# Kernel tuning notes

Measured on AMD Instinct MI355X. Metric: run time of the kernel, lower is better.

The kernel has to match this reference:

```python
import jax, jax.numpy as jnp
import numpy as np

COMMITMENT_COST = 0.25

def setup_inputs() -> dict:
    key = jax.random.key(0)
    k1, k2 = jax.random.split(key)
    z = jax.random.normal(k1, (8, 2048, 768), dtype=jnp.float32)
    # codebook initialized uniform(-1/K, 1/K) in the original; use same scale
    K = 2048
    emb = jax.random.uniform(k2, (K, 768), dtype=jnp.float32, minval=-1.0 / K, maxval=1.0 / K)
    return {"z": z, "emb": emb}

def reference(z, emb):
    B, S, D = z.shape
    z_flat = z.reshape(-1, D)                                   # [N, D]
    # squared-euclidean distances via expansion: ||z||^2 + ||e||^2 - 2 z e^T
    distances = (
        jnp.sum(z_flat * z_flat, axis=1, keepdims=True)
        + jnp.sum(emb * emb, axis=1)
        - 2.0 * jnp.matmul(z_flat, emb.T)
    )                                                           # [N, K]
    ids_flat = jnp.argmin(distances, axis=1)                    # [N]
    z_q = emb[ids_flat].reshape(z.shape)                        # gather + reshape
    concept_ids = ids_flat.reshape(B, S)
    # training path with use_ema=True: codebook_loss = 0, commitment term only.
    # NOTE: original (faithfully) computes mse(z.detach(), z_q) — grad flows to z_q.
    commitment_loss = jnp.mean((jax.lax.stop_gradient(z) - z_q) ** 2)
    vq_loss = COMMITMENT_COST * commitment_loss
    # straight-through estimator
    z_q_st = z + jax.lax.stop_gradient(z_q - z)
    return z_q_st, concept_ids, vq_loss
```

## Files before the change

kernel.cpp:

```cpp
#include <hip/hip_runtime.h>
#include <float.h>

typedef unsigned short ushort_t;
typedef unsigned int uint_t;

#define NROWS 16384
#define DDIM  768
#define KCODES 2048
#define NCB    16
#define MARGIN 8e-4f

__device__ __forceinline__ ushort_t f2bf(float x) {
    uint_t u = __float_as_uint(x);
    uint_t r = (u + 0x7fffu + ((u >> 16) & 1u)) >> 16;
    return (ushort_t)r;
}
__device__ __forceinline__ float bf2f(ushort_t h) {
    return __uint_as_float(((uint_t)h) << 16);
}

__global__ void ee_kernel(const float* __restrict__ emb, float* __restrict__ ee) {
    int c = blockIdx.x;
    const float* e = emb + (size_t)c * DDIM;
    int t = threadIdx.x;
    float s = 0.f;
    for (int i = t; i < DDIM; i += 256) { float v = e[i]; s += v * v; }
    for (int off = 32; off; off >>= 1) s += __shfl_down(s, off);
    __shared__ float red[4];
    if ((t & 63) == 0) red[t >> 6] = s;
    __syncthreads();
    if (t == 0) ee[c] = red[0] + red[1] + red[2] + red[3];
}

__global__ void zz_kernel(const float* __restrict__ z, float* __restrict__ zz) {
    const int t = threadIdx.x;
    const int row = blockIdx.x * 4 + (t >> 6);
    const int lane = t & 63;
    const float* zr = z + (size_t)row * DDIM;
    float s = 0.f;
    for (int i = lane; i < DDIM; i += 64) { float v = zr[i]; s += v * v; }
    for (int off = 32; off; off >>= 1) s += __shfl_down(s, off);
    if (lane == 0) zz[row] = s;
}

__global__ void conv_kernel(const float* __restrict__ src, ushort_t* __restrict__ dst) {
    const int i = blockIdx.x * 256 + threadIdx.x;
    const float4 v = ((const float4*)src)[i];
    ushort4 h;
    h.x = f2bf(v.x); h.y = f2bf(v.y); h.z = f2bf(v.z); h.w = f2bf(v.w);
    ((ushort4*)dst)[i] = h;
}

typedef __attribute__((ext_vector_type(8))) short bf16x8;
typedef __attribute__((ext_vector_type(4))) float f32x4;

__device__ __forceinline__ int swz(int r) { return (r & 3) ^ ((r >> 2) & 3); }

__global__ __launch_bounds__(256)
void mfma_kernel(const ushort_t* __restrict__ Ab, const ushort_t* __restrict__ Bb,
                 const float* __restrict__ ee, float* __restrict__ bmin,
                 float2* __restrict__ slots) {
    __shared__ ushort_t Als[128 * 32];
    __shared__ ushort_t Bls[128 * 32];
    __shared__ float rowmin[128];
    __shared__ int   rcnt[128];
    __shared__ float sval[128][8];
    __shared__ int   sidx[128][8];

    const int t = threadIdx.x;
    const int w = t >> 6, l = t & 63;
    const int bx = blockIdx.x & 127, by = blockIdx.x >> 7;
    const int row0 = bx << 7, col0 = by << 7;

    f32x4 acc[4][4];
    #pragma unroll
    for (int i = 0; i < 4; ++i)
        #pragma unroll
        for (int j = 0; j < 4; ++j) acc[i][j] = (f32x4){0.f, 0.f, 0.f, 0.f};

    const int sri  = l >> 2;
    const int slot = l & 3;
    const int rha = (w & 1) << 6;
    const int rhb = (w >> 1) << 6;

    for (int kt = 0; kt < 24; ++kt) {
        const int kb = kt << 5;
        __syncthreads();
        #pragma unroll
        for (int q = 0; q < 2; ++q) {
            const int r0 = ((w << 1) + q) << 4;
            const int ra = r0 + sri;
            const int c  = slot ^ swz(ra);
            const ushort_t* gpa = Ab + (size_t)(row0 + ra) * DDIM + kb + (c << 3);
            __builtin_amdgcn_global_load_lds(
                (const __attribute__((address_space(1))) void*)gpa,
                (__attribute__((address_space(3))) void*)((char*)Als + (r0 << 6)), 16, 0, 0);
            const ushort_t* gpb = Bb + (size_t)(col0 + ra) * DDIM + kb + (c << 3);
            __builtin_amdgcn_global_load_lds(
                (const __attribute__((address_space(1))) void*)gpb,
                (__attribute__((address_space(3))) void*)((char*)Bls + (r0 << 6)), 16, 0, 0);
        }
        __syncthreads();

        bf16x8 af[4], bfr[4];
        #pragma unroll
        for (int mi = 0; mi < 4; ++mi) {
            const int r = rha + (mi << 4) + (l & 15);
            const int s = (l >> 4) ^ swz(r);
            af[mi] = *(const bf16x8*)&Als[(r << 5) + (s << 3)];
        }
        #pragma unroll
        for (int ni = 0; ni < 4; ++ni) {
            const int r = rhb + (ni << 4) + (l & 15);
            const int s = (l >> 4) ^ swz(r);
            bfr[ni] = *(const bf16x8*)&Bls[(r << 5) + (s << 3)];
        }
        #pragma unroll
        for (int mi = 0; mi < 4; ++mi)
            #pragma unroll
            for (int ni = 0; ni < 4; ++ni)
                acc[mi][ni] = __builtin_amdgcn_mfma_f32_16x16x32_bf16(
                    af[mi], bfr[ni], acc[mi][ni], 0, 0, 0);
    }

    float ecv[4];
    #pragma unroll
    for (int ni = 0; ni < 4; ++ni) ecv[ni] = ee[col0 + rhb + (ni << 4) + (l & 15)];
    #pragma unroll
    for (int mi = 0; mi < 4; ++mi)
        #pragma unroll
        for (int ni = 0; ni < 4; ++ni)
            #pragma unroll
            for (int r = 0; r < 4; ++r)
                acc[mi][ni][r] = ecv[ni] - 2.0f * acc[mi][ni][r];

    float vmr[4][4];
    #pragma unroll
    for (int mi = 0; mi < 4; ++mi)
        #pragma unroll
        for (int r = 0; r < 4; ++r) {
            float v = fminf(fminf(acc[mi][0][r], acc[mi][1][r]),
                            fminf(acc[mi][2][r], acc[mi][3][r]));
            v = fminf(v, __shfl_xor(v, 1));
            v = fminf(v, __shfl_xor(v, 2));
            v = fminf(v, __shfl_xor(v, 4));
            v = fminf(v, __shfl_xor(v, 8));
            vmr[mi][r] = v;
        }

    if (t < 128) { rowmin[t] = FLT_MAX; rcnt[t] = 0; }
    __syncthreads();
    if (w < 2 && (l & 15) == 0) {
        #pragma unroll
        for (int mi = 0; mi < 4; ++mi)
            #pragma unroll
            for (int r = 0; r < 4; ++r)
                rowmin[rha + (mi << 4) + ((l >> 4) << 2) + r] = vmr[mi][r];
    }
    __syncthreads();
    if (w >= 2 && (l & 15) == 0) {
        #pragma unroll
        for (int mi = 0; mi < 4; ++mi)
            #pragma unroll
            for (int r = 0; r < 4; ++r) {
                const int m = rha + (mi << 4) + ((l >> 4) << 2) + r;
                rowmin[m] = fminf(rowmin[m], vmr[mi][r]);
            }
    }
    __syncthreads();

    #pragma unroll
    for (int mi = 0; mi < 4; ++mi)
        #pragma unroll
        for (int r = 0; r < 4; ++r) {
            const int m = rha + (mi << 4) + ((l >> 4) << 2) + r;
            const float lim = rowmin[m] + MARGIN;
            #pragma unroll
            for (int ni = 0; ni < 4; ++ni) {
                const float vv = acc[mi][ni][r];
                if (vv <= lim) {
                    const int p = atomicAdd(&rcnt[m], 1);
                    if (p < 8) {
                        sval[m][p] = vv;
                        sidx[m][p] = col0 + rhb + (ni << 4) + (l & 15);
                    }
                }
            }
        }
    __syncthreads();

    if (t < 128) {
        const int row = row0 + t;
        bmin[(size_t)by * NROWS + row] = rowmin[t];
        const int n = rcnt[t] < 8 ? rcnt[t] : 8;
        float2 rec[8];
        #pragma unroll
        for (int s2 = 0; s2 < 8; ++s2)
            rec[s2] = (s2 < n) ? make_float2(sval[t][s2], __int_as_float(sidx[t][s2]))
                               : make_float2(FLT_MAX, __int_as_float(0x7fffffff));
        float4* dst = (float4*)(slots + ((size_t)by * NROWS + row) * 8);
        dst[0] = make_float4(rec[0].x, rec[0].y, rec[1].x, rec[1].y);
        dst[1] = make_float4(rec[2].x, rec[2].y, rec[3].x, rec[3].y);
        dst[2] = make_float4(rec[4].x, rec[4].y, rec[5].x, rec[5].y);
        dst[3] = make_float4(rec[6].x, rec[6].y, rec[7].x, rec[7].y);
    }
}

__global__ __launch_bounds__(256)
void combine_select(const float* __restrict__ bmin, const float2* __restrict__ slots,
                    const float* __restrict__ ee, const float* __restrict__ zz,
                    const float* __restrict__ z, const float* __restrict__ emb,
                    float* __restrict__ ids_f32) {
    const int t = threadIdx.x;
    const int row = blockIdx.x * 4 + (t >> 6);
    const int l = t & 63;

    float v = (l < NCB) ? bmin[(size_t)l * NROWS + row] : FLT_MAX;
    v = fminf(v, __shfl_xor(v, 8));
    v = fminf(v, __shfl_xor(v, 4));
    v = fminf(v, __shfl_xor(v, 2));
    v = fminf(v, __shfl_xor(v, 1));
    const float T = __shfl(v, 0) + MARGIN;

    const int blk = l >> 2;
    const int s0 = (l << 1) & 7;
    const float2* sp = slots + ((size_t)blk * NROWS + row) * 8 + s0;
    const float2 a  = sp[0];
    const float2 b2 = sp[1];

    unsigned long long m0 = __ballot(a.x <= T);
    unsigned long long m1 = __ballot(b2.x <= T);

    const float zzr = zz[row];
    const float* zr = z + (size_t)row * DDIM;

    float bestd = FLT_MAX; int besti = 0x7fffffff;
    while (m0 | m1) {
        int j; float iv;
        if (m0) { j = __ffsll(m0) - 1; m0 &= m0 - 1; iv = a.y; }
        else    { j = __ffsll(m1) - 1; m1 &= m1 - 1; iv = b2.y; }
        const int idx = __float_as_int(__shfl(iv, j));
        const float* er = emb + (size_t)idx * DDIM;
        float p = 0.f;
        #pragma unroll
        for (int k = 0; k < 12; ++k) p += zr[l + 64 * k] * er[l + 64 * k];
        for (int off = 32; off; off >>= 1) p += __shfl_down(p, off);
        if (l == 0) {
            const float t1 = zzr + ee[idx];
            const float d  = t1 - 2.0f * p;
            if (d < bestd || (d == bestd && idx < besti)) { bestd = d; besti = idx; }
        }
    }
    if (l == 0) ids_f32[row] = (float)besti;
}

__global__ __launch_bounds__(256)
void gather_kernel(const float* __restrict__ z, const float* __restrict__ emb,
                   const float* __restrict__ ids_f32, float* __restrict__ out0,
                   float* __restrict__ part) {
    const int b = blockIdx.x;
    const int t = threadIdx.x;
    const int rl = t >> 4, c = t & 15;
    __shared__ int ids[16];
    if (t < 16) ids[t] = (int)ids_f32[b * 16 + t];
    __syncthreads();
    const int row = b * 16 + rl;
    const float4* zr = (const float4*)(z + (size_t)row * DDIM);
    float4* orow = (float4*)(out0 + (size_t)row * DDIM);
    const float4* er = (const float4*)(emb + (size_t)ids[rl] * DDIM);
    float s = 0.f;
    #pragma unroll
    for (int j = 0; j < 12; ++j) {
        const int i4 = c + 16 * j;
        const float4 zv = zr[i4];
        const float4 ev = er[i4];
        float4 o;
        o.x = zv.x + (ev.x - zv.x); o.y = zv.y + (ev.y - zv.y);
        o.z = zv.z + (ev.z - zv.z); o.w = zv.w + (ev.w - zv.w);
        orow[i4] = o;
        float dx = zv.x - ev.x, dy = zv.y - ev.y, dz = zv.z - ev.z, dw = zv.w - ev.w;
        s += dx * dx + dy * dy + dz * dz + dw * dw;
    }
    for (int off = 32; off; off >>= 1) s += __shfl_down(s, off);
    __shared__ float red[4];
    if ((t & 63) == 0) red[t >> 6] = s;
    __syncthreads();
    if (t == 0) part[b] = red[0] + red[1] + red[2] + red[3];
}

__global__ void loss_kernel(const float* __restrict__ part, float* __restrict__ out_loss) {
    const int t = threadIdx.x;
    double s = 0.0;
    for (int i = t; i < 1024; i += 256) s += (double)part[i];
    for (int off = 32; off; off >>= 1) s += __shfl_down(s, off);
    __shared__ double red[4];
    if ((t & 63) == 0) red[t >> 6] = s;
    __syncthreads();
    if (t == 0) {
        const double total = red[0] + red[1] + red[2] + red[3];
        out_loss[0] = (float)(0.25 * (total / (double)((size_t)NROWS * DDIM)));
    }
}

#define BM 32
#define BN 128
#define BKS 32
#define SPLITC 2
#define CODES_PER_BLOCK (KCODES / SPLITC)
#define NCHUNK (CODES_PER_BLOCK / BN)
#define NSTAGE (DDIM / BKS)
#define APADR 33
#define BPADC 132

__global__ __launch_bounds__(256)
void argmin_kernel(const float* __restrict__ z, const float* __restrict__ emb,
                   const float* __restrict__ ee, const float* __restrict__ zz,
                   float* __restrict__ pval, int* __restrict__ pidx) {
    __shared__ float Af[BKS][APADR];
    __shared__ float Bf[BKS][BPADC];
    __shared__ float cval[BM][33];
    __shared__ int   cidx[BM][33];
    __shared__ float zzs[BM];
    const int t = threadIdx.x;
    const int part = blockIdx.x & (SPLITC - 1);
    const int rb = blockIdx.x >> 1;
    const int row0 = rb * BM;
    const int cbase = part * CODES_PER_BLOCK;
    const int tx = t & 31, ty = t >> 5;
    const int sr = t >> 3;
    const int sk = 4 * (t & 7);
    if (t < BM) zzs[t] = zz[row0 + t];
    float bv[4]; int bi[4];
    #pragma unroll
    for (int i = 0; i < 4; ++i) { bv[i] = FLT_MAX; bi[i] = 0x7fffffff; }
    const float* zt = z + (size_t)(row0 + sr) * DDIM;
    for (int chunk = 0; chunk < NCHUNK; ++chunk) {
        const int c0 = cbase + chunk * BN;
        const float* ebase = emb + (size_t)(c0 + sr) * DDIM;
        float acc[4][4];
        #pragma unroll
        for (int i = 0; i < 4; ++i)
            #pragma unroll
            for (int j = 0; j < 4; ++j) acc[i][j] = 0.f;
        float4 pa = *(const float4*)&zt[sk];
        float4 pb[4];
        #pragma unroll
        for (int m = 0; m < 4; ++m) pb[m] = *(const float4*)&ebase[(size_t)(32 * m) * DDIM + sk];
        for (int s = 0; s < NSTAGE; ++s) {
            __syncthreads();
            Af[sk + 0][sr] = pa.x; Af[sk + 1][sr] = pa.y;
            Af[sk + 2][sr] = pa.z; Af[sk + 3][sr] = pa.w;
            #pragma unroll
            for (int m = 0; m < 4; ++m) {
                Bf[sk + 0][sr + 32 * m] = pb[m].x;
                Bf[sk + 1][sr + 32 * m] = pb[m].y;
                Bf[sk + 2][sr + 32 * m] = pb[m].z;
                Bf[sk + 3][sr + 32 * m] = pb[m].w;
            }
            __syncthreads();
            if (s + 1 < NSTAGE) {
                const int k1 = (s + 1) * BKS + sk;
                pa = *(const float4*)&zt[k1];
                #pragma unroll
                for (int m = 0; m < 4; ++m)
                    pb[m] = *(const float4*)&ebase[(size_t)(32 * m) * DDIM + k1];
            }
            #pragma unroll
            for (int kk = 0; kk < BKS; ++kk) {
                const float4 a4 = *(const float4*)&Af[kk][4 * ty];
                const float4 b4 = *(const float4*)&Bf[kk][4 * tx];
                const float aa[4] = {a4.x, a4.y, a4.z, a4.w};
                const float bb[4] = {b4.x, b4.y, b4.z, b4.w};
                #pragma unroll
                for (int i = 0; i < 4; ++i)
                    #pragma unroll
                    for (int j = 0; j < 4; ++j) acc[i][j] += aa[i] * bb[j];
            }
        }
        const float4 e4 = *(const float4*)&ee[c0 + 4 * tx];
        const float eev[4] = {e4.x, e4.y, e4.z, e4.w};
        #pragma unroll
        for (int i = 0; i < 4; ++i) {
            const float zzr = zzs[4 * ty + i];
            #pragma unroll
            for (int j = 0; j < 4; ++j) {
                const int code = c0 + 4 * tx + j;
                const float t1 = zzr + eev[j];
                const float d  = t1 - 2.0f * acc[i][j];
                if (d < bv[i] || (d == bv[i] && code < bi[i])) { bv[i] = d; bi[i] = code; }
            }
        }
    }
    __syncthreads();
    #pragma unroll
    for (int i = 0; i < 4; ++i) { cval[4 * ty + i][tx] = bv[i]; cidx[4 * ty + i][tx] = bi[i]; }
    __syncthreads();
    if (t < BM) {
        float v = FLT_MAX; int id = 0x7fffffff;
        #pragma unroll
        for (int x = 0; x < 32; ++x) {
            const float cv = cval[t][x]; const int ci = cidx[t][x];
            if (cv < v || (cv == v && ci < id)) { v = cv; id = ci; }
        }
        pval[part * NROWS + row0 + t] = v;
        pidx[part * NROWS + row0 + t] = id;
    }
}

__global__ void combine_kernel(const float* __restrict__ pval, const int* __restrict__ pidx,
                               float* __restrict__ ids_f32) {
    const int r = blockIdx.x * 256 + threadIdx.x;
    float v = pval[r];           int id = pidx[r];
    const float v1 = pval[NROWS + r]; const int i1 = pidx[NROWS + r];
    if (v1 < v || (v1 == v && i1 < id)) { v = v1; id = i1; }
    ids_f32[r] = (float)id;
}

#define EE_OFF   0
#define ZZ_OFF   8192
#define PART_OFF 73728
#define PV_OFF   81920
#define EH_OFF   81920
#define ZH_OFF   (EH_OFF + (size_t)KCODES * DDIM * 2)
#define BMIN_OFF (ZH_OFF + (size_t)NROWS * DDIM * 2)
#define SLOT_OFF (BMIN_OFF + (size_t)NCB * NROWS * 4)
#define WS_NEED  (SLOT_OFF + (size_t)NCB * NROWS * 8 * 8)

extern "C" void kernel_launch(void* const* d_in, const int* in_sizes, int n_in,
                              void* d_out, int out_size, void* d_ws, size_t ws_size,
                              hipStream_t stream) {
    const float* z   = (const float*)d_in[0];
    const float* emb = (const float*)d_in[1];

    float* out0     = (float*)d_out;
    float* out_ids  = out0 + (size_t)NROWS * DDIM;
    float* out_loss = out_ids + NROWS;

    char* ws = (char*)d_ws;
    float* ee   = (float*)(ws + EE_OFF);
    float* zzws = (float*)(ws + ZZ_OFF);
    float* part = (float*)(ws + PART_OFF);

    ee_kernel<<<KCODES, 256, 0, stream>>>(emb, ee);
    zz_kernel<<<NROWS / 4, 256, 0, stream>>>(z, zzws);

    if (ws_size >= WS_NEED) {
        ushort_t* Eh   = (ushort_t*)(ws + EH_OFF);
        ushort_t* Zh   = (ushort_t*)(ws + ZH_OFF);
        float*    bmin = (float*)(ws + BMIN_OFF);
        float2*   slot = (float2*)(ws + SLOT_OFF);
        conv_kernel<<<(KCODES * DDIM / 4) / 256, 256, 0, stream>>>(emb, Eh);
        conv_kernel<<<(NROWS * DDIM / 4) / 256, 256, 0, stream>>>(z, Zh);
        mfma_kernel<<<(NROWS / 128) * NCB, 256, 0, stream>>>(Zh, Eh, ee, bmin, slot);
        combine_select<<<NROWS / 4, 256, 0, stream>>>(bmin, slot, ee, zzws, z, emb, out_ids);
    } else {
        float* pval = (float*)(ws + PV_OFF);
        int*   pidx = (int*)(ws + PV_OFF + 131072);
        argmin_kernel<<<(NROWS / BM) * SPLITC, 256, 0, stream>>>(z, emb, ee, zzws, pval, pidx);
        combine_kernel<<<NROWS / 256, 256, 0, stream>>>(pval, pidx, out_ids);
    }

    gather_kernel<<<NROWS / 16, 256, 0, stream>>>(z, emb, out_ids, out0, part);
    loss_kernel<<<1, 256, 0, stream>>>(part, out_loss);
}
```

Measured before the change: 257.4 us.

## Fuse bf16 conversion into norm kernels, fuse gather into select, deepen K-tile

Merges the bf16 conversion of emb and z into the norm-computing prep kernels, so each input is read once instead of twice. Folds the straight-through gather and per-row loss into the candidate-rescoring kernel, which removes a separate pass that re-read z and emb. The MFMA kernel now stages 64 K-elements per barrier pair instead of 32, halving the number of sync iterations, and reuses one shared-memory buffer for the epilogue arrays. The cost is a larger LDS footprint (32 KB), which may lower occupancy, plus an extra barrier before that reuse.

```diff
diff --git a/kernel.cpp b/kernel.cpp
--- a/kernel.cpp
+++ b/kernel.cpp
@@ -19,7 +19,8 @@
     return __uint_as_float(((uint_t)h) << 16);
 }
 
-__global__ void ee_kernel(const float* __restrict__ emb, float* __restrict__ ee) {
+__global__ void prep_emb(const float* __restrict__ emb, float* __restrict__ ee,
+                         ushort_t* __restrict__ Eh) {
     int c = blockIdx.x;
     const float* e = emb + (size_t)c * DDIM;
     int t = threadIdx.x;
@@ -30,9 +31,16 @@
     if ((t & 63) == 0) red[t >> 6] = s;
     __syncthreads();
     if (t == 0) ee[c] = red[0] + red[1] + red[2] + red[3];
-}
-
-__global__ void zz_kernel(const float* __restrict__ z, float* __restrict__ zz) {
+    if (t < 192) {
+        const float4 v = ((const float4*)e)[t];
+        ushort4 h;
+        h.x = f2bf(v.x); h.y = f2bf(v.y); h.z = f2bf(v.z); h.w = f2bf(v.w);
+        ((ushort4*)(Eh + (size_t)c * DDIM))[t] = h;
+    }
+}
+
+__global__ void prep_z(const float* __restrict__ z, float* __restrict__ zz,
+                       ushort_t* __restrict__ Zh) {
     const int t = threadIdx.x;
     const int row = blockIdx.x * 4 + (t >> 6);
     const int lane = t & 63;
@@ -41,14 +49,16 @@
     for (int i = lane; i < DDIM; i += 64) { float v = zr[i]; s += v * v; }
     for (int off = 32; off; off >>= 1) s += __shfl_down(s, off);
     if (lane == 0) zz[row] = s;
-}
-
-__global__ void conv_kernel(const float* __restrict__ src, ushort_t* __restrict__ dst) {
-    const int i = blockIdx.x * 256 + threadIdx.x;
-    const float4 v = ((const float4*)src)[i];
-    ushort4 h;
-    h.x = f2bf(v.x); h.y = f2bf(v.y); h.z = f2bf(v.z); h.w = f2bf(v.w);
-    ((ushort4*)dst)[i] = h;
+    const float4* zr4 = (const float4*)zr;
+    ushort4* dh = (ushort4*)(Zh + (size_t)row * DDIM);
+    #pragma unroll
+    for (int j = 0; j < 3; ++j) {
+        const int i4 = lane + 64 * j;
+        const float4 v = zr4[i4];
+        ushort4 h;
+        h.x = f2bf(v.x); h.y = f2bf(v.y); h.z = f2bf(v.z); h.w = f2bf(v.w);
+        dh[i4] = h;
+    }
 }
 
 typedef __attribute__((ext_vector_type(8))) short bf16x8;
@@ -60,12 +70,13 @@
 void mfma_kernel(const ushort_t* __restrict__ Ab, const ushort_t* __restrict__ Bb,
                  const float* __restrict__ ee, float* __restrict__ bmin,
                  float2* __restrict__ slots) {
-    __shared__ ushort_t Als[128 * 32];
-    __shared__ ushort_t Bls[128 * 32];
-    __shared__ float rowmin[128];
-    __shared__ int   rcnt[128];
-    __shared__ float sval[128][8];
-    __shared__ int   sidx[128][8];
+    __shared__ __align__(16) char smem[32768];
+    ushort_t* Als = (ushort_t*)smem;
+    ushort_t* Bls = (ushort_t*)(smem + 16384);
+    float* rowmin = (float*)smem;
+    int*   rcnt   = (int*)(smem + 512);
+    float (*sval)[8] = (float(*)[8])(smem + 1024);
+    int   (*sidx)[8] = (int(*)[8])(smem + 5120);
 
     const int t = threadIdx.x;
     const int w = t >> 6, l = t & 63;
@@ -83,45 +94,55 @@
     const int rha = (w & 1) << 6;
     const int rhb = (w >> 1) << 6;
 
-    for (int kt = 0; kt < 24; ++kt) {
-        const int kb = kt << 5;
+    for (int kt = 0; kt < 12; ++kt) {
+        const int kb = kt << 6;
         __syncthreads();
         #pragma unroll
-        for (int q = 0; q < 2; ++q) {
-            const int r0 = ((w << 1) + q) << 4;
-            const int ra = r0 + sri;
-            const int c  = slot ^ swz(ra);
-            const ushort_t* gpa = Ab + (size_t)(row0 + ra) * DDIM + kb + (c << 3);
-            __builtin_amdgcn_global_load_lds(
-                (const __attribute__((address_space(1))) void*)gpa,
-                (__attribute__((address_space(3))) void*)((char*)Als + (r0 << 6)), 16, 0, 0);
-            const ushort_t* gpb = Bb + (size_t)(col0 + ra) * DDIM + kb + (c << 3);
-            __builtin_amdgcn_global_load_lds(
-                (const __attribute__((address_space(1))) void*)gpb,
-                (__attribute__((address_space(3))) void*)((char*)Bls + (r0 << 6)), 16, 0, 0);
+        for (int s = 0; s < 2; ++s) {
+            #pragma unroll
+            for (int q = 0; q < 2; ++q) {
+                const int r0 = ((w << 1) + q) << 4;
+                const int ra = r0 + sri;
+                const int c  = slot ^ swz(ra);
+                const int kk = kb + (s << 5) + (c << 3);
+                const ushort_t* gpa = Ab + (size_t)(row0 + ra) * DDIM + kk;
+                __builtin_amdgcn_global_load_lds(
+                    (const __attribute__((address_space(1))) void*)gpa,
+                    (__attribute__((address_space(3))) void*)(smem + (s << 13) + (r0 << 6)),
+                    16, 0, 0);
+                const ushort_t* gpb = Bb + (size_t)(col0 + ra) * DDIM + kk;
+                __builtin_amdgcn_global_load_lds(
+                    (const __attribute__((address_space(1))) void*)gpb,
+                    (__attribute__((address_space(3))) void*)(smem + 16384 + (s << 13) + (r0 << 6)),
+                    16, 0, 0);
+            }
         }
         __syncthreads();
 
-        bf16x8 af[4], bfr[4];
-        #pragma unroll
-        for (int mi = 0; mi < 4; ++mi) {
-            const int r = rha + (mi << 4) + (l & 15);
-            const int s = (l >> 4) ^ swz(r);
-            af[mi] = *(const bf16x8*)&Als[(r << 5) + (s << 3)];
-        }
-        #pragma unroll
-        for (int ni = 0; ni < 4; ++ni) {
-            const int r = rhb + (ni << 4) + (l & 15);
-            const int s = (l >> 4) ^ swz(r);
-            bfr[ni] = *(const bf16x8*)&Bls[(r << 5) + (s << 3)];
-        }
-        #pragma unroll
-        for (int mi = 0; mi < 4; ++mi)
-            #pragma unroll
-            for (int ni = 0; ni < 4; ++ni)
-                acc[mi][ni] = __builtin_amdgcn_mfma_f32_16x16x32_bf16(
-                    af[mi], bfr[ni], acc[mi][ni], 0, 0, 0);
-    }
+        #pragma unroll
+        for (int s = 0; s < 2; ++s) {
+            bf16x8 af[4], bfr[4];
+            #pragma unroll
+            for (int mi = 0; mi < 4; ++mi) {
+                const int r = rha + (mi << 4) + (l & 15);
+                const int sw = (l >> 4) ^ swz(r);
+                af[mi] = *(const bf16x8*)&Als[(s << 12) + (r << 5) + (sw << 3)];
+            }
+            #pragma unroll
+            for (int ni = 0; ni < 4; ++ni) {
+                const int r = rhb + (ni << 4) + (l & 15);
+                const int sw = (l >> 4) ^ swz(r);
+                bfr[ni] = *(const bf16x8*)&Bls[(s << 12) + (r << 5) + (sw << 3)];
+            }
+            #pragma unroll
+            for (int mi = 0; mi < 4; ++mi)
+                #pragma unroll
+                for (int ni = 0; ni < 4; ++ni)
+                    acc[mi][ni] = __builtin_amdgcn_mfma_f32_16x16x32_bf16(
+                        af[mi], bfr[ni], acc[mi][ni], 0, 0, 0);
+        }
+    }
+    __syncthreads();
 
     float ecv[4];
     #pragma unroll
@@ -207,10 +228,11 @@
 }
 
 __global__ __launch_bounds__(256)
-void combine_select(const float* __restrict__ bmin, const float2* __restrict__ slots,
-                    const float* __restrict__ ee, const float* __restrict__ zz,
-                    const float* __restrict__ z, const float* __restrict__ emb,
-                    float* __restrict__ ids_f32) {
+void combine_select_gather(const float* __restrict__ bmin, const float2* __restrict__ slots,
+                           const float* __restrict__ ee, const float* __restrict__ zz,
+                           const float* __restrict__ z, const float* __restrict__ emb,
+                           float* __restrict__ ids_f32, float* __restrict__ out0,
+                           float* __restrict__ rowloss) {
     const int t = threadIdx.x;
     const int row = blockIdx.x * 4 + (t >> 6);
     const int l = t & 63;
@@ -251,7 +273,180 @@
             if (d < bestd || (d == bestd && idx < besti)) { bestd = d; besti = idx; }
         }
     }
-    if (l == 0) ids_f32[row] = (float)besti;
+    const int bi = __shfl(besti, 0);
+    if (l == 0) ids_f32[row] = (float)bi;
+
+    const float4* zr4 = (const float4*)zr;
+    const float4* er4 = (const float4*)(emb + (size_t)bi * DDIM);
+    float4* o4 = (float4*)(out0 + (size_t)row * DDIM);
+    float s = 0.f;
+    #pragma unroll
+    for (int j = 0; j < 3; ++j) {
+        const int i4 = l + 64 * j;
+        const float4 zv = zr4[i4];
+        const float4 ev = er4[i4];
+        float4 o;
+        o.x = zv.x + (ev.x - zv.x); o.y = zv.y + (ev.y - zv.y);
+        o.z = zv.z + (ev.z - zv.z); o.w = zv.w + (ev.w - zv.w);
+        o4[i4] = o;
+        const float dx = zv.x - ev.x, dy = zv.y - ev.y;
+        const float dz = zv.z - ev.z, dw = zv.w - ev.w;
+        s += dx * dx + dy * dy + dz * dz + dw * dw;
+    }
+    for (int off = 32; off; off >>= 1) s += __shfl_down(s, off);
+    if (l == 0) rowloss[row] = s;
+}
+
+__global__ void loss16k_kernel(const float* __restrict__ rowloss, float* __restrict__ out_loss) {
+    const int t = threadIdx.x;
+    double s = 0.0;
+    for (int i = t; i < NROWS; i += 256) s += (double)rowloss[i];
+    for (int off = 32; off; off >>= 1) s += __shfl_down(s, off);
+    __shared__ double red[4];
+    if ((t & 63) == 0) red[t >> 6] = s;
+    __syncthreads();
+    if (t == 0) {
+        const double total = red[0] + red[1] + red[2] + red[3];
+        out_loss[0] = (float)(0.25 * (total / (double)((size_t)NROWS * DDIM)));
+    }
+}
+
+__global__ void ee_kernel(const float* __restrict__ emb, float* __restrict__ ee) {
+    int c = blockIdx.x;
+    const float* e = emb + (size_t)c * DDIM;
+    int t = threadIdx.x;
+    float s = 0.f;
+    for (int i = t; i < DDIM; i += 256) { float v = e[i]; s += v * v; }
+    for (int off = 32; off; off >>= 1) s += __shfl_down(s, off);
+    __shared__ float red[4];
+    if ((t & 63) == 0) red[t >> 6] = s;
+    __syncthreads();
+    if (t == 0) ee[c] = red[0] + red[1] + red[2] + red[3];
+}
+
+__global__ void zz_kernel(const float* __restrict__ z, float* __restrict__ zz) {
+    const int t = threadIdx.x;
+    const int row = blockIdx.x * 4 + (t >> 6);
+    const int lane = t & 63;
+    const float* zr = z + (size_t)row * DDIM;
+    float s = 0.f;
+    for (int i = lane; i < DDIM; i += 64) { float v = zr[i]; s += v * v; }
+    for (int off = 32; off; off >>= 1) s += __shfl_down(s, off);
+    if (lane == 0) zz[row] = s;
+}
+
+#define BM 32
+#define BN 128
+#define BKS 32
+#define SPLITC 2
+#define CODES_PER_BLOCK (KCODES / SPLITC)
+#define NCHUNK (CODES_PER_BLOCK / BN)
+#define NSTAGE (DDIM / BKS)
+#define APADR 33
+#define BPADC 132
+
+__global__ __launch_bounds__(256)
+void argmin_kernel(const float* __restrict__ z, const float* __restrict__ emb,
+                   const float* __restrict__ ee, const float* __restrict__ zz,
+                   float* __restrict__ pval, int* __restrict__ pidx) {
+    __shared__ float Af[BKS][APADR];
+    __shared__ float Bf[BKS][BPADC];
+    __shared__ float cval[BM][33];
+    __shared__ int   cidx[BM][33];
+    __shared__ float zzs[BM];
+    const int t = threadIdx.x;
+    const int part = blockIdx.x & (SPLITC - 1);
+    const int rb = blockIdx.x >> 1;
+    const int row0 = rb * BM;
+    const int cbase = part * CODES_PER_BLOCK;
+    const int tx = t & 31, ty = t >> 5;
+    const int sr = t >> 3;
+    const int sk = 4 * (t & 7);
+    if (t < BM) zzs[t] = zz[row0 + t];
+    float bv[4]; int bi[4];
+    #pragma unroll
+    for (int i = 0; i < 4; ++i) { bv[i] = FLT_MAX; bi[i] = 0x7fffffff; }
+    const float* zt = z + (size_t)(row0 + sr) * DDIM;
+    for (int chunk = 0; chunk < NCHUNK; ++chunk) {
+        const int c0 = cbase + chunk * BN;
+        const float* ebase = emb + (size_t)(c0 + sr) * DDIM;
+        float acc[4][4];
+        #pragma unroll
+        for (int i = 0; i < 4; ++i)
+            #pragma unroll
+            for (int j = 0; j < 4; ++j) acc[i][j] = 0.f;
+        float4 pa = *(const float4*)&zt[sk];
+        float4 pb[4];
+        #pragma unroll
+        for (int m = 0; m < 4; ++m) pb[m] = *(const float4*)&ebase[(size_t)(32 * m) * DDIM + sk];
+        for (int s = 0; s < NSTAGE; ++s) {
+            __syncthreads();
+            Af[sk + 0][sr] = pa.x; Af[sk + 1][sr] = pa.y;
+            Af[sk + 2][sr] = pa.z; Af[sk + 3][sr] = pa.w;
+            #pragma unroll
+            for (int m = 0; m < 4; ++m) {
+                Bf[sk + 0][sr + 32 * m] = pb[m].x;
+                Bf[sk + 1][sr + 32 * m] = pb[m].y;
+                Bf[sk + 2][sr + 32 * m] = pb[m].z;
+                Bf[sk + 3][sr + 32 * m] = pb[m].w;
+            }
+            __syncthreads();
+            if (s + 1 < NSTAGE) {
+                const int k1 = (s + 1) * BKS + sk;
+                pa = *(const float4*)&zt[k1];
+                #pragma unroll
+                for (int m = 0; m < 4; ++m)
+                    pb[m] = *(const float4*)&ebase[(size_t)(32 * m) * DDIM + k1];
+            }
+            #pragma unroll
+            for (int kk = 0; kk < BKS; ++kk) {
+                const float4 a4 = *(const float4*)&Af[kk][4 * ty];
+                const float4 b4 = *(const float4*)&Bf[kk][4 * tx];
+                const float aa[4] = {a4.x, a4.y, a4.z, a4.w};
+                const float bb[4] = {b4.x, b4.y, b4.z, b4.w};
+                #pragma unroll
+                for (int i = 0; i < 4; ++i)
+                    #pragma unroll
+                    for (int j = 0; j < 4; ++j) acc[i][j] += aa[i] * bb[j];
+            }
+        }
+        const float4 e4 = *(const float4*)&ee[c0 + 4 * tx];
+        const float eev[4] = {e4.x, e4.y, e4.z, e4.w};
+        #pragma unroll
+        for (int i = 0; i < 4; ++i) {
+            const float zzr = zzs[4 * ty + i];
+            #pragma unroll
+            for (int j = 0; j < 4; ++j) {
+                const int code = c0 + 4 * tx + j;
+                const float t1 = zzr + eev[j];
+                const float d  = t1 - 2.0f * acc[i][j];
+                if (d < bv[i] || (d == bv[i] && code < bi[i])) { bv[i] = d; bi[i] = code; }
+            }
+        }
+    }
+    __syncthreads();
+    #pragma unroll
+    for (int i = 0; i < 4; ++i) { cval[4 * ty + i][tx] = bv[i]; cidx[4 * ty + i][tx] = bi[i]; }
+    __syncthreads();
+    if (t < BM) {
+        float v = FLT_MAX; int id = 0x7fffffff;
+        #pragma unroll
+        for (int x = 0; x < 32; ++x) {
+            const float cv = cval[t][x]; const int ci = cidx[t][x];
+            if (cv < v || (cv == v && ci < id)) { v = cv; id = ci; }
+        }
+        pval[part * NROWS + row0 + t] = v;
+        pidx[part * NROWS + row0 + t] = id;
+    }
+}
+
+__global__ void combine_kernel(const float* __restrict__ pval, const int* __restrict__ pidx,
+                               float* __restrict__ ids_f32) {
+    const int r = blockIdx.x * 256 + threadIdx.x;
+    float v = pval[r];           int id = pidx[r];
+    const float v1 = pval[NROWS + r]; const int i1 = pidx[NROWS + r];
+    if (v1 < v || (v1 == v && i1 < id)) { v = v1; id = i1; }
+    ids_f32[r] = (float)id;
 }
 
 __global__ __launch_bounds__(256)
@@ -302,129 +497,15 @@
     }
 }
 
-#define BM 32
-#define BN 128
-#define BKS 32
-#define SPLITC 2
-#define CODES_PER_BLOCK (KCODES / SPLITC)
-#define NCHUNK (CODES_PER_BLOCK / BN)
-#define NSTAGE (DDIM / BKS)
-#define APADR 33
-#define BPADC 132
-
-__global__ __launch_bounds__(256)
-void argmin_kernel(const float* __restrict__ z, const float* __restrict__ emb,
-                   const float* __restrict__ ee, const float* __restrict__ zz,
-                   float* __restrict__ pval, int* __restrict__ pidx) {
-    __shared__ float Af[BKS][APADR];
-    __shared__ float Bf[BKS][BPADC];
-    __shared__ float cval[BM][33];
-    __shared__ int   cidx[BM][33];
-    __shared__ float zzs[BM];
-    const int t = threadIdx.x;
-    const int part = blockIdx.x & (SPLITC - 1);
-    const int rb = blockIdx.x >> 1;
-    const int row0 = rb * BM;
-    const int cbase = part * CODES_PER_BLOCK;
-    const int tx = t & 31, ty = t >> 5;
-    const int sr = t >> 3;
-    const int sk = 4 * (t & 7);
-    if (t < BM) zzs[t] = zz[row0 + t];
-    float bv[4]; int bi[4];
-    #pragma unroll
-    for (int i = 0; i < 4; ++i) { bv[i] = FLT_MAX; bi[i] = 0x7fffffff; }
-    const float* zt = z + (size_t)(row0 + sr) * DDIM;
-    for (int chunk = 0; chunk < NCHUNK; ++chunk) {
-        const int c0 = cbase + chunk * BN;
-        const float* ebase = emb + (size_t)(c0 + sr) * DDIM;
-        float acc[4][4];
-        #pragma unroll
-        for (int i = 0; i < 4; ++i)
-            #pragma unroll
-            for (int j = 0; j < 4; ++j) acc[i][j] = 0.f;
-        float4 pa = *(const float4*)&zt[sk];
-        float4 pb[4];
-        #pragma unroll
-        for (int m = 0; m < 4; ++m) pb[m] = *(const float4*)&ebase[(size_t)(32 * m) * DDIM + sk];
-        for (int s = 0; s < NSTAGE; ++s) {
-            __syncthreads();
-            Af[sk + 0][sr] = pa.x; Af[sk + 1][sr] = pa.y;
-            Af[sk + 2][sr] = pa.z; Af[sk + 3][sr] = pa.w;
-            #pragma unroll
-            for (int m = 0; m < 4; ++m) {
-                Bf[sk + 0][sr + 32 * m] = pb[m].x;
-                Bf[sk + 1][sr + 32 * m] = pb[m].y;
-                Bf[sk + 2][sr + 32 * m] = pb[m].z;
-                Bf[sk + 3][sr + 32 * m] = pb[m].w;
-            }
-            __syncthreads();
-            if (s + 1 < NSTAGE) {
-                const int k1 = (s + 1) * BKS + sk;
-                pa = *(const float4*)&zt[k1];
-                #pragma unroll
-                for (int m = 0; m < 4; ++m)
-                    pb[m] = *(const float4*)&ebase[(size_t)(32 * m) * DDIM + k1];
-            }
-            #pragma unroll
-            for (int kk = 0; kk < BKS; ++kk) {
-                const float4 a4 = *(const float4*)&Af[kk][4 * ty];
-                const float4 b4 = *(const float4*)&Bf[kk][4 * tx];
-                const float aa[4] = {a4.x, a4.y, a4.z, a4.w};
-                const float bb[4] = {b4.x, b4.y, b4.z, b4.w};
-                #pragma unroll
-                for (int i = 0; i < 4; ++i)
-                    #pragma unroll
-                    for (int j = 0; j < 4; ++j) acc[i][j] += aa[i] * bb[j];
-            }
-        }
-        const float4 e4 = *(const float4*)&ee[c0 + 4 * tx];
-        const float eev[4] = {e4.x, e4.y, e4.z, e4.w};
-        #pragma unroll
-        for (int i = 0; i < 4; ++i) {
-            const float zzr = zzs[4 * ty + i];
-            #pragma unroll
-            for (int j = 0; j < 4; ++j) {
-                const int code = c0 + 4 * tx + j;
-                const float t1 = zzr + eev[j];
-                const float d  = t1 - 2.0f * acc[i][j];
-                if (d < bv[i] || (d == bv[i] && code < bi[i])) { bv[i] = d; bi[i] = code; }
-            }
-        }
-    }
-    __syncthreads();
-    #pragma unroll
-    for (int i = 0; i < 4; ++i) { cval[4 * ty + i][tx] = bv[i]; cidx[4 * ty + i][tx] = bi[i]; }
-    __syncthreads();
-    if (t < BM) {
-        float v = FLT_MAX; int id = 0x7fffffff;
-        #pragma unroll
-        for (int x = 0; x < 32; ++x) {
-            const float cv = cval[t][x]; const int ci = cidx[t][x];
-            if (cv < v || (cv == v && ci < id)) { v = cv; id = ci; }
-        }
-        pval[part * NROWS + row0 + t] = v;
-        pidx[part * NROWS + row0 + t] = id;
-    }
-}
-
-__global__ void combine_kernel(const float* __restrict__ pval, const int* __restrict__ pidx,
-                               float* __restrict__ ids_f32) {
-    const int r = blockIdx.x * 256 + threadIdx.x;
-    float v = pval[r];           int id = pidx[r];
-    const float v1 = pval[NROWS + r]; const int i1 = pidx[NROWS + r];
-    if (v1 < v || (v1 == v && i1 < id)) { v = v1; id = i1; }
-    ids_f32[r] = (float)id;
-}
-
 #define EE_OFF   0
 #define ZZ_OFF   8192
-#define PART_OFF 73728
-#define PV_OFF   81920
-#define EH_OFF   81920
+#define RL_OFF   73728
+#define EH_OFF   139264
 #define ZH_OFF   (EH_OFF + (size_t)KCODES * DDIM * 2)
 #define BMIN_OFF (ZH_OFF + (size_t)NROWS * DDIM * 2)
 #define SLOT_OFF (BMIN_OFF + (size_t)NCB * NROWS * 4)
 #define WS_NEED  (SLOT_OFF + (size_t)NCB * NROWS * 8 * 8)
+#define PV_OFF   81920
 
 extern "C" void kernel_launch(void* const* d_in, const int* in_sizes, int n_in,
                               void* d_out, int out_size, void* d_ws, size_t ws_size,
@@ -439,27 +520,28 @@
     char* ws = (char*)d_ws;
     float* ee   = (float*)(ws + EE_OFF);
     float* zzws = (float*)(ws + ZZ_OFF);
-    float* part = (float*)(ws + PART_OFF);
-
-    ee_kernel<<<KCODES, 256, 0, stream>>>(emb, ee);
-    zz_kernel<<<NROWS / 4, 256, 0, stream>>>(z, zzws);
 
     if (ws_size >= WS_NEED) {
         ushort_t* Eh   = (ushort_t*)(ws + EH_OFF);
         ushort_t* Zh   = (ushort_t*)(ws + ZH_OFF);
         float*    bmin = (float*)(ws + BMIN_OFF);
         float2*   slot = (float2*)(ws + SLOT_OFF);
-        conv_kernel<<<(KCODES * DDIM / 4) / 256, 256, 0, stream>>>(emb, Eh);
-        conv_kernel<<<(NROWS * DDIM / 4) / 256, 256, 0, stream>>>(z, Zh);
+        float*    rl   = (float*)(ws + RL_OFF);
+        prep_emb<<<KCODES, 256, 0, stream>>>(emb, ee, Eh);
+        prep_z<<<NROWS / 4, 256, 0, stream>>>(z, zzws, Zh);
         mfma_kernel<<<(NROWS / 128) * NCB, 256, 0, stream>>>(Zh, Eh, ee, bmin, slot);
-        combine_select<<<NROWS / 4, 256, 0, stream>>>(bmin, slot, ee, zzws, z, emb, out_ids);
+        combine_select_gather<<<NROWS / 4, 256, 0, stream>>>(bmin, slot, ee, zzws, z, emb,
+                                                             out_ids, out0, rl);
+        loss16k_kernel<<<1, 256, 0, stream>>>(rl, out_loss);
     } else {
+        float* part = (float*)(ws + RL_OFF);
         float* pval = (float*)(ws + PV_OFF);
         int*   pidx = (int*)(ws + PV_OFF + 131072);
+        ee_kernel<<<KCODES, 256, 0, stream>>>(emb, ee);
+        zz_kernel<<<NROWS / 4, 256, 0, stream>>>(z, zzws);
         argmin_kernel<<<(NROWS / BM) * SPLITC, 256, 0, stream>>>(z, emb, ee, zzws, pval, pidx);
         combine_kernel<<<NROWS / 256, 256, 0, stream>>>(pval, pidx, out_ids);
-    }
-
-    gather_kernel<<<NROWS / 16, 256, 0, stream>>>(z, emb, out_ids, out0, part);
-    loss_kernel<<<1, 256, 0, stream>>>(part, out_loss);
-}
+        gather_kernel<<<NROWS / 16, 256, 0, stream>>>(z, emb, out_ids, out0, part);
+        loss_kernel<<<1, 256, 0, stream>>>(part, out_loss);
+    }
+}
```

After: 249.3 us. -3.1%, faster.
